# Kernel optimization log

Measured on AMD Instinct MI355X. Metric: run time of the kernel, lower is better.

Reference implementation:

```python
import jax, jax.numpy as jnp
import numpy as np

NUM_SPARSE = 26
VOCAB = 100000
EMB = 64
B = 2048
DENSE = 13
NUM_FEA = NUM_SPARSE + 1  # 26 embeddings + bottom-MLP output


def _xavier(key, shape):
    fan_in, fan_out = shape[0], shape[1]
    lim = jnp.sqrt(6.0 / (fan_in + fan_out))
    return jax.random.uniform(key, shape, jnp.float32, -lim, lim)


def setup_inputs() -> dict:
    key = jax.random.key(0)
    ks = jax.random.split(key, 20)
    inp = {
        "dense": jax.random.normal(ks[0], (B, DENSE), jnp.float32),
        "cat_idx": jax.random.randint(ks[1], (B, NUM_SPARSE), 0, VOCAB, jnp.int32),
        # stacked EmbeddingBag tables (all same vocab -> one [26, V, 64] tensor)
        "tables": _xavier(ks[2], (VOCAB, EMB))[None] * jnp.ones((NUM_SPARSE, 1, 1), jnp.float32) * 0
                  + jax.random.normal(ks[3], (NUM_SPARSE, VOCAB, EMB), jnp.float32) * 0.01,
        # bottom MLP: 13 -> 512 -> 256 -> 64
        "bw0": _xavier(ks[4], (DENSE, 512)), "bb0": jnp.zeros((512,), jnp.float32),
        "bw1": _xavier(ks[5], (512, 256)),   "bb1": jnp.zeros((256,), jnp.float32),
        "bw2": _xavier(ks[6], (256, EMB)),   "bb2": jnp.zeros((EMB,), jnp.float32),
        # top MLP: 415 -> 1024 -> 512 -> 256 -> 1
        "tw0": _xavier(ks[7], (EMB + NUM_FEA * (NUM_FEA - 1) // 2, 1024)), "tb0": jnp.zeros((1024,), jnp.float32),
        "tw1": _xavier(ks[8], (1024, 512)),  "tb1": jnp.zeros((512,), jnp.float32),
        "tw2": _xavier(ks[9], (512, 256)),   "tb2": jnp.zeros((256,), jnp.float32),
        "tw3": _xavier(ks[10], (256, 1)),    "tb3": jnp.zeros((1,), jnp.float32),
    }
    return inp


def reference(dense, cat_idx, tables, bw0, bb0, bw1, bb1, bw2, bb2,
              tw0, tb0, tw1, tb1, tw2, tb2, tw3, tb3):
    # bottom MLP on dense features -> [B, EMB]
    h = jax.nn.relu(dense @ bw0 + bb0)
    h = jax.nn.relu(h @ bw1 + bb1)
    bot = jax.nn.relu(h @ bw2 + bb2)

    # EmbeddingBag (single index per bag, sum mode == plain gather): [B, 26, EMB]
    feat_ids = jnp.arange(NUM_SPARSE)[None, :]  # [1, 26]
    emb = tables[feat_ids, cat_idx]             # [B, 26, EMB]

    # dot interaction: batched Gram matrix then lower-triangular gather
    T = jnp.concatenate([bot[:, None, :], emb], axis=1)  # [B, 27, EMB]
    Z = jnp.einsum("bif,bjf->bij", T, T)                  # [B, 27, 27]
    li, lj = np.tril_indices(NUM_FEA, k=-1)               # 351 pairs
    Zflat = Z[:, li, lj]                                  # [B, 351]

    R = jnp.concatenate([bot, Zflat], axis=1)             # [B, 415]

    # top MLP
    r = jax.nn.relu(R @ tw0 + tb0)
    r = jax.nn.relu(r @ tw1 + tb1)
    r = jax.nn.relu(r @ tw2 + tb2)
    out = jax.nn.sigmoid(r @ tw3 + tb3)                   # [B, 1]
    return out
```

## Files before the change

kernel.cpp:

```cpp
#include <hip/hip_runtime.h>
#include <hip/hip_bf16.h>


#define BATCH 2048
#define VOCAB 100000
#define NSPARSE 26
#define NFEA 27
#define NPAIR 351
#define RLD 512

typedef __attribute__((ext_vector_type(8))) __bf16 bf16x8;
typedef __attribute__((ext_vector_type(4))) float f32x4;
typedef __hip_bfloat16 bf16;

#define GLOAD16(g, l)                                                          \
    __builtin_amdgcn_global_load_lds(                                          \
        (const __attribute__((address_space(1))) unsigned int*)(g),            \
        (__attribute__((address_space(3))) unsigned int*)(l), 16, 0, 0)

template<int BK>
__device__ __forceinline__ int swz(int row, int s) {
    return (BK == 128) ? (s ^ (row & 15))
         : (BK == 64)  ? (s ^ (row & 7))
                       : (s ^ ((row >> 1) & 3));
}

template<int BK, int WR, int WC, int MREP, int NREP, bool DENSEPAD>
__global__ __launch_bounds__(256) void gemm_bf16(
    const void* __restrict__ Araw,
    const bf16* __restrict__ Wt,
    const float* __restrict__ bias,
    bf16* __restrict__ C,
    int M, int N, int K, int ldC)
{
    constexpr int BM    = WR * MREP * 16;
    constexpr int BN    = WC * NREP * 16;
    constexpr int ROWB  = BK * 2;
    constexpr int SLOTS = BK / 8;
    constexpr int KKS   = BK / 32;
    constexpr int PA    = BM * SLOTS / 256;
    constexpr int PB    = BN * SLOTS / 256;

    __shared__ __align__(16) bf16 As[BM * BK];
    __shared__ __align__(16) bf16 Bs[BN * BK];

    const int t   = threadIdx.x;
    const int nbn = N / BN;
    const int bm  = blockIdx.x / nbn;
    const int bn  = blockIdx.x % nbn;
    const int row0 = bm * BM, n0 = bn * BN;

    const int wid  = t >> 6, lane = t & 63;
    const int wr   = wid / WC, wc = wid % WC;
    const int lr   = lane & 15;
    const int q    = lane >> 4;
    const int sslot = t % SLOTS;

    const bf16* Ab[PA];
    const bf16* Bb[PB];
#pragma unroll
    for (int p = 0; p < PA; ++p) {
        const int r = (p * 256 + t) / SLOTS;
        if (!DENSEPAD)
            Ab[p] = (const bf16*)Araw + (size_t)(row0 + r) * K +
                    swz<BK>(r, sslot) * 8;
    }
#pragma unroll
    for (int p = 0; p < PB; ++p) {
        const int r = (p * 256 + t) / SLOTS;
        Bb[p] = Wt + (size_t)(n0 + r) * K + swz<BK>(r, sslot) * 8;
    }

    f32x4 acc[MREP][NREP] = {};

    for (int k0 = 0; k0 < K; k0 += BK) {
        if constexpr (DENSEPAD) {
            const float* Df = (const float*)Araw;
#pragma unroll
            for (int idx = t; idx < BM * 32; idx += 256) {
                const int r = idx >> 5, c = idx & 31;
                const float v = (c < 13) ? Df[(size_t)(row0 + r) * 13 + c] : 0.f;
                As[r * 32 + swz<32>(r, c >> 3) * 8 + (c & 7)] =
                    __float2bfloat16(v);
            }
        } else {
#pragma unroll
            for (int p = 0; p < PA; ++p)
                GLOAD16(Ab[p] + k0, (char*)As + (p * 256 + t) * 16);
        }
#pragma unroll
        for (int p = 0; p < PB; ++p)
            GLOAD16(Bb[p] + k0, (char*)Bs + (p * 256 + t) * 16);
        __syncthreads();

        bf16x8 af[KKS][MREP], bfr[KKS][NREP];
#pragma unroll
        for (int kk = 0; kk < KKS; ++kk) {
#pragma unroll
            for (int m = 0; m < MREP; ++m) {
                const int r = wr * MREP * 16 + 16 * m + lr;
                af[kk][m] = *(const bf16x8*)((const char*)As + r * ROWB +
                                             swz<BK>(r, kk * 4 + q) * 16);
            }
#pragma unroll
            for (int n = 0; n < NREP; ++n) {
                const int r = wc * NREP * 16 + 16 * n + lr;
                bfr[kk][n] = *(const bf16x8*)((const char*)Bs + r * ROWB +
                                              swz<BK>(r, kk * 4 + q) * 16);
            }
        }
#pragma unroll
        for (int kk = 0; kk < KKS; ++kk)
#pragma unroll
            for (int m = 0; m < MREP; ++m)
#pragma unroll
                for (int n = 0; n < NREP; ++n)
                    acc[m][n] = __builtin_amdgcn_mfma_f32_16x16x32_bf16(
                        af[kk][m], bfr[kk][n], acc[m][n], 0, 0, 0);
        __syncthreads();
    }

#pragma unroll
    for (int n = 0; n < NREP; ++n) {
        const int col = n0 + wc * NREP * 16 + 16 * n + lr;
        const float bv = bias[col];
#pragma unroll
        for (int m = 0; m < MREP; ++m) {
#pragma unroll
            for (int i = 0; i < 4; ++i) {
                const int row = row0 + wr * MREP * 16 + 16 * m + q * 4 + i;
                float v = fmaxf(acc[m][n][i] + bv, 0.f);
                C[(size_t)row * ldC + col] = __float2bfloat16(v);
            }
        }
    }
}

__global__ __launch_bounds__(256) void top2_kernel(
    const bf16* __restrict__ A,
    const bf16* __restrict__ Wt,
    const float* __restrict__ bias,
    const float* __restrict__ w3,
    const float* __restrict__ b3,
    float* __restrict__ out)
{
    constexpr int BK = 64, BM = 32, BN = 256, K = 512;
    constexpr int SLOTS = 8, KKS = 2, PA = 1, PB = 8;

    __shared__ __align__(16) bf16 As[BM * BK];
    __shared__ __align__(16) bf16 Bs[BN * BK];
    __shared__ float rsum[BM];

    const int t = threadIdx.x;
    const int row0 = blockIdx.x * BM;
    const int wc = t >> 6, lane = t & 63;
    const int lr = lane & 15, q = lane >> 4;
    const int sslot = t % SLOTS;

    const bf16* Ab[PA];
    const bf16* Bb[PB];
#pragma unroll
    for (int p = 0; p < PA; ++p) {
        const int r = (p * 256 + t) / SLOTS;
        Ab[p] = A + (size_t)(row0 + r) * K + swz<BK>(r, sslot) * 8;
    }
#pragma unroll
    for (int p = 0; p < PB; ++p) {
        const int r = (p * 256 + t) / SLOTS;
        Bb[p] = Wt + (size_t)r * K + swz<BK>(r, sslot) * 8;
    }

    f32x4 acc[2][4] = {};

    for (int k0 = 0; k0 < K; k0 += BK) {
#pragma unroll
        for (int p = 0; p < PA; ++p)
            GLOAD16(Ab[p] + k0, (char*)As + (p * 256 + t) * 16);
#pragma unroll
        for (int p = 0; p < PB; ++p)
            GLOAD16(Bb[p] + k0, (char*)Bs + (p * 256 + t) * 16);
        __syncthreads();

        bf16x8 af[KKS][2], bfr[KKS][4];
#pragma unroll
        for (int kk = 0; kk < KKS; ++kk) {
#pragma unroll
            for (int m = 0; m < 2; ++m) {
                const int r = 16 * m + lr;
                af[kk][m] = *(const bf16x8*)((const char*)As + r * 128 +
                                             swz<BK>(r, kk * 4 + q) * 16);
            }
#pragma unroll
            for (int n = 0; n < 4; ++n) {
                const int r = wc * 64 + 16 * n + lr;
                bfr[kk][n] = *(const bf16x8*)((const char*)Bs + r * 128 +
                                              swz<BK>(r, kk * 4 + q) * 16);
            }
        }
#pragma unroll
        for (int kk = 0; kk < KKS; ++kk)
#pragma unroll
            for (int m = 0; m < 2; ++m)
#pragma unroll
                for (int n = 0; n < 4; ++n)
                    acc[m][n] = __builtin_amdgcn_mfma_f32_16x16x32_bf16(
                        af[kk][m], bfr[kk][n], acc[m][n], 0, 0, 0);
        __syncthreads();
    }

    if (t < BM) rsum[t] = 0.f;
    __syncthreads();

#pragma unroll
    for (int m = 0; m < 2; ++m) {
#pragma unroll
        for (int i = 0; i < 4; ++i) {
            float val = 0.f;
#pragma unroll
            for (int n = 0; n < 4; ++n) {
                const int col = wc * 64 + 16 * n + lr;
                val += fmaxf(acc[m][n][i] + bias[col], 0.f) * w3[col];
            }
            val += __shfl_xor(val, 1);
            val += __shfl_xor(val, 2);
            val += __shfl_xor(val, 4);
            val += __shfl_xor(val, 8);
            if (lr == 0) atomicAdd(&rsum[16 * m + q * 4 + i], val);
        }
    }
    __syncthreads();
    if (t < BM)
        out[row0 + t] = 1.f / (1.f + expf(-(rsum[t] + b3[0])));
}

struct WConvArgs {
    const float* src[6];
    bf16*        dst[6];
    int K[6], N[6], Kp[6], t0[7];
};

__global__ __launch_bounds__(256) void wconv_kernel(WConvArgs a)
{
    __shared__ float Ts[32][33];
    int w = 0;
    while (w < 5 && (int)blockIdx.x >= a.t0[w + 1]) ++w;
    const int rel = blockIdx.x - a.t0[w];
    const int K = a.K[w], N = a.N[w], Kp = a.Kp[w];
    const int nbn = N >> 5;
    const int tk = rel / nbn, tn = rel % nbn;
    const int tx = threadIdx.x & 31, ty = threadIdx.x >> 5;

    const float* src = a.src[w];
    bf16* dst = a.dst[w];

#pragma unroll
    for (int rr = 0; rr < 4; ++rr) {
        const int k = tk * 32 + ty + rr * 8;
        const int n = tn * 32 + tx;
        Ts[ty + rr * 8][tx] = (k < K) ? src[(size_t)k * N + n] : 0.f;
    }
    __syncthreads();
#pragma unroll
    for (int rr = 0; rr < 4; ++rr) {
        const int n = tn * 32 + ty + rr * 8;
        const int kp = tk * 32 + tx;
        dst[(size_t)n * Kp + kp] = __float2bfloat16(Ts[tx][ty + rr * 8]);
    }
}

__global__ __launch_bounds__(256) void interact_kernel(
    const int* __restrict__ cat_idx, const float* __restrict__ tables,
    bf16* __restrict__ R)
{
    __shared__ float T[NFEA][64 + 1];

    const int b    = blockIdx.x;
    const int t    = threadIdx.x;
    const int g    = t >> 6;
    const int lane = t & 63;
    bf16* Rrow = R + (size_t)b * RLD;

    for (int f = g; f < NFEA; f += 4) {
        if (f == 0) {
            T[0][lane] = __bfloat162float(Rrow[lane]);
        } else {
            const int j   = f - 1;
            const int idx = cat_idx[b * NSPARSE + j];
            T[f][lane] = tables[((size_t)j * VOCAB + idx) * 64 + lane];
        }
    }
    __syncthreads();

    if (t < RLD - 415) Rrow[415 + t] = __float2bfloat16(0.f);

    for (int p = t; p < NPAIR; p += 256) {
        int i = (int)((1.0f + sqrtf(1.0f + 8.0f * (float)p)) * 0.5f);
        while (i * (i - 1) / 2 > p) --i;
        while ((i + 1) * i / 2 <= p) ++i;
        const int j = p - i * (i - 1) / 2;
        float s = 0.f;
#pragma unroll 16
        for (int k = 0; k < 64; ++k) s += T[i][k] * T[j][k];
        Rrow[64 + p] = __float2bfloat16(s);
    }
}

extern "C" void kernel_launch(void* const* d_in, const int* in_sizes, int n_in,
                              void* d_out, int out_size, void* d_ws, size_t ws_size,
                              hipStream_t stream)
{
    const float* dense   = (const float*)d_in[0];
    const int*   cat_idx = (const int*)  d_in[1];
    const float* tables  = (const float*)d_in[2];
    const float* bw0 = (const float*)d_in[3];
    const float* bb0 = (const float*)d_in[4];
    const float* bw1 = (const float*)d_in[5];
    const float* bb1 = (const float*)d_in[6];
    const float* bw2 = (const float*)d_in[7];
    const float* bb2 = (const float*)d_in[8];
    const float* tw0 = (const float*)d_in[9];
    const float* tb0 = (const float*)d_in[10];
    const float* tw1 = (const float*)d_in[11];
    const float* tb1 = (const float*)d_in[12];
    const float* tw2 = (const float*)d_in[13];
    const float* tb2 = (const float*)d_in[14];
    const float* tw3 = (const float*)d_in[15];
    const float* tb3 = (const float*)d_in[16];

    bf16* p = (bf16*)d_ws;
    bf16* h0   = p; p += (size_t)BATCH * 512;
    bf16* h1   = p; p += (size_t)BATCH * 256;
    bf16* R    = p; p += (size_t)BATCH * RLD;
    bf16* r0   = p; p += (size_t)BATCH * 1024;
    bf16* r1   = p; p += (size_t)BATCH * 512;
    bf16* bw0t = p; p += 512 * 32;
    bf16* bw1t = p; p += 256 * 512;
    bf16* bw2t = p; p += 64 * 256;
    bf16* tw0t = p; p += 1024 * RLD;
    bf16* tw1t = p; p += 512 * 1024;
    bf16* tw2t = p; p += 256 * 512;
    float* out = (float*)d_out;

    WConvArgs wa;
    wa.src[0] = bw0;  wa.dst[0] = bw0t; wa.K[0] = 13;   wa.N[0] = 512;  wa.Kp[0] = 32;
    wa.src[1] = bw1;  wa.dst[1] = bw1t; wa.K[1] = 512;  wa.N[1] = 256;  wa.Kp[1] = 512;
    wa.src[2] = bw2;  wa.dst[2] = bw2t; wa.K[2] = 256;  wa.N[2] = 64;   wa.Kp[2] = 256;
    wa.src[3] = tw0;  wa.dst[3] = tw0t; wa.K[3] = 415;  wa.N[3] = 1024; wa.Kp[3] = RLD;
    wa.src[4] = tw1;  wa.dst[4] = tw1t; wa.K[4] = 1024; wa.N[4] = 512;  wa.Kp[4] = 1024;
    wa.src[5] = tw2;  wa.dst[5] = tw2t; wa.K[5] = 512;  wa.N[5] = 256;  wa.Kp[5] = 512;
    int tiles = 0;
    for (int w = 0; w < 6; ++w) {
        wa.t0[w] = tiles;
        tiles += (wa.Kp[w] >> 5) * (wa.N[w] >> 5);
    }
    wa.t0[6] = tiles;

    wconv_kernel<<<tiles, 256, 0, stream>>>(wa);

    gemm_bf16<32, 2, 2, 2, 2, true ><<<(BATCH / 64) * (512 / 64), 256, 0, stream>>>(
        dense, bw0t, bb0, h0, BATCH, 512, 32, 512);
    gemm_bf16<128, 2, 2, 2, 2, false><<<(BATCH / 64) * (256 / 64), 256, 0, stream>>>(
        h0, bw1t, bb1, h1, BATCH, 256, 512, 256);
    gemm_bf16<128, 2, 2, 2, 2, false><<<(BATCH / 64) * (64 / 64), 256, 0, stream>>>(
        h1, bw2t, bb2, R, BATCH, 64, 256, RLD);

    interact_kernel<<<BATCH, 256, 0, stream>>>(cat_idx, tables, R);

    gemm_bf16<128, 2, 2, 2, 2, false><<<(BATCH / 64) * (1024 / 64), 256, 0, stream>>>(
        R, tw0t, tb0, r0, BATCH, 1024, RLD, 1024);
    gemm_bf16<128, 2, 2, 2, 2, false><<<(BATCH / 64) * (512 / 64), 256, 0, stream>>>(
        r0, tw1t, tb1, r1, BATCH, 512, 1024, 512);
    top2_kernel<<<BATCH / 32, 256, 0, stream>>>(r1, tw2t, tb2, tw3, tb3, out);
}
```

Before: 63.75 us.

## Merge gather, weight conversion and first bottom GEMM into one multi-role kernel

```diff
diff --git a/kernel.cpp b/kernel.cpp
--- a/kernel.cpp
+++ b/kernel.cpp
@@ -25,12 +25,205 @@
                        : (s ^ ((row >> 1) & 3));
 }
 
-template<int BK, int WR, int WC, int MREP, int NREP, bool DENSEPAD>
+struct Mix1Args {
+    const int* cat; const float* tables; bf16* R; bf16* Tg;
+    const float* wsrc[5]; bf16* wdst[5];
+    int wK[5], wN[5], wKp[5], wt0[6];
+    const float* dense; const float* bw0; const float* bb0; bf16* h0;
+};
+
+__device__ void gather_role(const Mix1Args& a, char* ldsc, int gb)
+{
+    float (*T)[NFEA][65] = (float(*)[NFEA][65])ldsc;
+    const int t  = threadIdx.x;
+    const int b0 = gb * 4;
+
+    for (int l = t; l < 4 * NSPARSE * 16; l += 256) {
+        const int r = l / (NSPARSE * 16), rem = l % (NSPARSE * 16);
+        const int j = rem >> 4, c = (rem & 15) * 4;
+        const int idx = a.cat[(b0 + r) * NSPARSE + j];
+        const float4 v =
+            *(const float4*)&a.tables[((size_t)j * VOCAB + idx) * 64 + c];
+        float* dst = &T[r][j + 1][c];
+        dst[0] = v.x; dst[1] = v.y; dst[2] = v.z; dst[3] = v.w;
+    }
+    for (int z = t; z < 4 * (RLD - 415); z += 256) {
+        const int r = z / (RLD - 415), c = z % (RLD - 415);
+        a.R[(size_t)(b0 + r) * RLD + 415 + c] = __float2bfloat16(0.f);
+    }
+    __syncthreads();
+
+    for (int l = t; l < 4 * NSPARSE * 8; l += 256) {
+        const int r = l / (NSPARSE * 8), rem = l % (NSPARSE * 8);
+        const int j = rem >> 3, k8 = rem & 7;
+        union { bf16 h[8]; bf16x8 v; } pk;
+#pragma unroll
+        for (int u = 0; u < 8; ++u)
+            pk.h[u] = __float2bfloat16(T[r][j + 1][k8 * 8 + u]);
+        *(bf16x8*)&a.Tg[((size_t)(b0 + r) * NSPARSE + j) * 64 + k8 * 8] = pk.v;
+    }
+
+    for (int task = t; task < 4 * NPAIR; task += 256) {
+        const int r = task / NPAIR, p = task % NPAIR;
+        int i = (int)((1.0f + sqrtf(1.0f + 8.0f * (float)p)) * 0.5f);
+        while (i * (i - 1) / 2 > p) --i;
+        while ((i + 1) * i / 2 <= p) ++i;
+        const int j = p - i * (i - 1) / 2;
+        if (j == 0) continue;
+        float s = 0.f;
+#pragma unroll 16
+        for (int k = 0; k < 64; ++k) s += T[r][i][k] * T[r][j][k];
+        a.R[(size_t)(b0 + r) * RLD + 64 + p] = __float2bfloat16(s);
+    }
+}
+
+__device__ void wconv_role(const Mix1Args& a, char* ldsc, int wb)
+{
+    float (*Ts)[33] = (float(*)[33])ldsc;
+    int w = 0;
+    while (w < 4 && wb >= a.wt0[w + 1]) ++w;
+    const int rel = wb - a.wt0[w];
+    const int K = a.wK[w], N = a.wN[w], Kp = a.wKp[w];
+    const int nbn = N >> 5;
+    const int tk = rel / nbn, tn = rel % nbn;
+    const int tx = threadIdx.x & 31, ty = threadIdx.x >> 5;
+
+    const float* src = a.wsrc[w];
+    bf16* dst = a.wdst[w];
+#pragma unroll
+    for (int rr = 0; rr < 4; ++rr) {
+        const int k = tk * 32 + ty + rr * 8, n = tn * 32 + tx;
+        Ts[ty + rr * 8][tx] = (k < K) ? src[(size_t)k * N + n] : 0.f;
+    }
+    __syncthreads();
+#pragma unroll
+    for (int rr = 0; rr < 4; ++rr) {
+        const int n = tn * 32 + ty + rr * 8, kp = tk * 32 + tx;
+        dst[(size_t)n * Kp + kp] = __float2bfloat16(Ts[tx][ty + rr * 8]);
+    }
+}
+
+__device__ void gemm0_role(const Mix1Args& a, char* ldsc, int mb)
+{
+    bf16* As = (bf16*)ldsc;
+    bf16* Bs = (bf16*)(ldsc + 4096);
+    constexpr int N = 512;
+
+    const int t = threadIdx.x;
+    const int nbn = N >> 6;
+    const int bm = mb / nbn, bn = mb % nbn;
+    const int row0 = bm << 6, n0 = bn << 6;
+    const int wid = t >> 6, lane = t & 63;
+    const int wr = wid >> 1, wc = wid & 1;
+    const int lr = lane & 15, q = lane >> 4;
+
+    for (int idx = t; idx < 64 * 32; idx += 256) {
+        const int r = idx >> 5, c = idx & 31;
+        const float v = (c < 13) ? a.dense[(size_t)(row0 + r) * 13 + c] : 0.f;
+        As[r * 32 + swz<32>(r, c >> 3) * 8 + (c & 7)] = __float2bfloat16(v);
+    }
+    for (int idx = t; idx < 64 * 32; idx += 256) {
+        const int r = idx >> 5, c = idx & 31;
+        const float v = (c < 13) ? a.bw0[(size_t)c * N + n0 + r] : 0.f;
+        Bs[r * 32 + swz<32>(r, c >> 3) * 8 + (c & 7)] = __float2bfloat16(v);
+    }
+    __syncthreads();
+
+    f32x4 acc[2][2] = {};
+    bf16x8 af[2], bfr[2];
+#pragma unroll
+    for (int m = 0; m < 2; ++m) {
+        const int r = wr * 32 + 16 * m + lr;
+        af[m] = *(const bf16x8*)((const char*)As + r * 64 + swz<32>(r, q) * 16);
+    }
+#pragma unroll
+    for (int n = 0; n < 2; ++n) {
+        const int r = wc * 32 + 16 * n + lr;
+        bfr[n] = *(const bf16x8*)((const char*)Bs + r * 64 + swz<32>(r, q) * 16);
+    }
+#pragma unroll
+    for (int m = 0; m < 2; ++m)
+#pragma unroll
+        for (int n = 0; n < 2; ++n)
+            acc[m][n] = __builtin_amdgcn_mfma_f32_16x16x32_bf16(
+                af[m], bfr[n], acc[m][n], 0, 0, 0);
+
+#pragma unroll
+    for (int n = 0; n < 2; ++n) {
+        const int col = n0 + wc * 32 + 16 * n + lr;
+        const float bv = a.bb0[col];
+#pragma unroll
+        for (int m = 0; m < 2; ++m) {
+#pragma unroll
+            for (int i = 0; i < 4; ++i) {
+                const int row = row0 + wr * 32 + 16 * m + q * 4 + i;
+                a.h0[(size_t)row * 512 + col] =
+                    __float2bfloat16(fmaxf(acc[m][n][i] + bv, 0.f));
+            }
+        }
+    }
+}
+
+__global__ __launch_bounds__(256) void mix1_kernel(Mix1Args a)
+{
+    __shared__ __align__(16) char lds[28288];
+    const int bid = blockIdx.x;
+    if (bid < 512)            gather_role(a, lds, bid);
+    else if (bid < 1808)      wconv_role(a, lds, bid - 512);
+    else                      gemm0_role(a, lds, bid - 1808);
+}
+
+__global__ __launch_bounds__(256) void botmix_kernel(
+    const bf16* __restrict__ h1, const bf16* __restrict__ bw2t,
+    const float* __restrict__ bb2, const bf16* __restrict__ Tg,
+    bf16* __restrict__ R)
+{
+    __shared__ bf16  h1s[8][256];
+    __shared__ float bots[8][64];
+    const int t  = threadIdx.x;
+    const int b0 = blockIdx.x * 8;
+
+    {   const int r = t >> 5, c = (t & 31) * 8;
+        *(bf16x8*)&h1s[r][c] = *(const bf16x8*)&h1[(size_t)(b0 + r) * 256 + c]; }
+    __syncthreads();
+
+    for (int o = t; o < 512; o += 256) {
+        const int r = o >> 6, n = o & 63;
+        float s = bb2[n];
+        const bf16* wrow = bw2t + (size_t)n * 256;
+#pragma unroll 8
+        for (int k = 0; k < 256; k += 8) {
+            const bf16x8 hv = *(const bf16x8*)&h1s[r][k];
+            const bf16x8 wv = *(const bf16x8*)&wrow[k];
+#pragma unroll
+            for (int u = 0; u < 8; ++u)
+                s += (float)hv[u] * (float)wv[u];
+        }
+        s = fmaxf(s, 0.f);
+        bots[r][n] = s;
+        R[(size_t)(b0 + r) * RLD + n] = __float2bfloat16(s);
+    }
+    __syncthreads();
+
+    if (t < 8 * NSPARSE) {
+        const int r = t / NSPARSE, iz = t % NSPARSE, i = iz + 1;
+        const bf16* tgrow = Tg + ((size_t)(b0 + r) * NSPARSE + iz) * 64;
+        float s = 0.f;
+#pragma unroll
+        for (int k8 = 0; k8 < 8; ++k8) {
+            const bf16x8 ev = *(const bf16x8*)&tgrow[k8 * 8];
+#pragma unroll
+            for (int u = 0; u < 8; ++u)
+                s += (float)ev[u] * bots[r][k8 * 8 + u];
+        }
+        R[(size_t)(b0 + r) * RLD + 64 + i * (i - 1) / 2] = __float2bfloat16(s);
+    }
+}
+
+template<int BK, int WR, int WC, int MREP, int NREP>
 __global__ __launch_bounds__(256) void gemm_bf16(
-    const void* __restrict__ Araw,
-    const bf16* __restrict__ Wt,
-    const float* __restrict__ bias,
-    bf16* __restrict__ C,
+    const bf16* __restrict__ A, const bf16* __restrict__ Wt,
+    const float* __restrict__ bias, bf16* __restrict__ C,
     int M, int N, int K, int ldC)
 {
     constexpr int BM    = WR * MREP * 16;
@@ -61,9 +254,7 @@
 #pragma unroll
     for (int p = 0; p < PA; ++p) {
         const int r = (p * 256 + t) / SLOTS;
-        if (!DENSEPAD)
-            Ab[p] = (const bf16*)Araw + (size_t)(row0 + r) * K +
-                    swz<BK>(r, sslot) * 8;
+        Ab[p] = A + (size_t)(row0 + r) * K + swz<BK>(r, sslot) * 8;
     }
 #pragma unroll
     for (int p = 0; p < PB; ++p) {
@@ -74,20 +265,9 @@
     f32x4 acc[MREP][NREP] = {};
 
     for (int k0 = 0; k0 < K; k0 += BK) {
-        if constexpr (DENSEPAD) {
-            const float* Df = (const float*)Araw;
-#pragma unroll
-            for (int idx = t; idx < BM * 32; idx += 256) {
-                const int r = idx >> 5, c = idx & 31;
-                const float v = (c < 13) ? Df[(size_t)(row0 + r) * 13 + c] : 0.f;
-                As[r * 32 + swz<32>(r, c >> 3) * 8 + (c & 7)] =
-                    __float2bfloat16(v);
-            }
-        } else {
-#pragma unroll
-            for (int p = 0; p < PA; ++p)
-                GLOAD16(Ab[p] + k0, (char*)As + (p * 256 + t) * 16);
-        }
+#pragma unroll
+        for (int p = 0; p < PA; ++p)
+            GLOAD16(Ab[p] + k0, (char*)As + (p * 256 + t) * 16);
 #pragma unroll
         for (int p = 0; p < PB; ++p)
             GLOAD16(Bb[p] + k0, (char*)Bs + (p * 256 + t) * 16);
@@ -129,26 +309,23 @@
 #pragma unroll
             for (int i = 0; i < 4; ++i) {
                 const int row = row0 + wr * MREP * 16 + 16 * m + q * 4 + i;
-                float v = fmaxf(acc[m][n][i] + bv, 0.f);
-                C[(size_t)row * ldC + col] = __float2bfloat16(v);
+                C[(size_t)row * ldC + col] =
+                    __float2bfloat16(fmaxf(acc[m][n][i] + bv, 0.f));
             }
         }
     }
 }
 
 __global__ __launch_bounds__(256) void top2_kernel(
-    const bf16* __restrict__ A,
-    const bf16* __restrict__ Wt,
-    const float* __restrict__ bias,
-    const float* __restrict__ w3,
-    const float* __restrict__ b3,
-    float* __restrict__ out)
-{
-    constexpr int BK = 64, BM = 32, BN = 256, K = 512;
+    const bf16* __restrict__ A, const bf16* __restrict__ Wt,
+    const float* __restrict__ bias, const float* __restrict__ w3,
+    const float* __restrict__ b3, float* __restrict__ out)
+{
+    constexpr int BK = 64, BM = 32, K = 512;
     constexpr int SLOTS = 8, KKS = 2, PA = 1, PB = 8;
 
     __shared__ __align__(16) bf16 As[BM * BK];
-    __shared__ __align__(16) bf16 Bs[BN * BK];
+    __shared__ __align__(16) bf16 Bs[256 * BK];
     __shared__ float rsum[BM];
 
     const int t = threadIdx.x;
@@ -231,78 +408,6 @@
     __syncthreads();
     if (t < BM)
         out[row0 + t] = 1.f / (1.f + expf(-(rsum[t] + b3[0])));
-}
-
-struct WConvArgs {
-    const float* src[6];
-    bf16*        dst[6];
-    int K[6], N[6], Kp[6], t0[7];
-};
-
-__global__ __launch_bounds__(256) void wconv_kernel(WConvArgs a)
-{
-    __shared__ float Ts[32][33];
-    int w = 0;
-    while (w < 5 && (int)blockIdx.x >= a.t0[w + 1]) ++w;
-    const int rel = blockIdx.x - a.t0[w];
-    const int K = a.K[w], N = a.N[w], Kp = a.Kp[w];
-    const int nbn = N >> 5;
-    const int tk = rel / nbn, tn = rel % nbn;
-    const int tx = threadIdx.x & 31, ty = threadIdx.x >> 5;
-
-    const float* src = a.src[w];
-    bf16* dst = a.dst[w];
-
-#pragma unroll
-    for (int rr = 0; rr < 4; ++rr) {
-        const int k = tk * 32 + ty + rr * 8;
-        const int n = tn * 32 + tx;
-        Ts[ty + rr * 8][tx] = (k < K) ? src[(size_t)k * N + n] : 0.f;
-    }
-    __syncthreads();
-#pragma unroll
-    for (int rr = 0; rr < 4; ++rr) {
-        const int n = tn * 32 + ty + rr * 8;
-        const int kp = tk * 32 + tx;
-        dst[(size_t)n * Kp + kp] = __float2bfloat16(Ts[tx][ty + rr * 8]);
-    }
-}
-
-__global__ __launch_bounds__(256) void interact_kernel(
-    const int* __restrict__ cat_idx, const float* __restrict__ tables,
-    bf16* __restrict__ R)
-{
-    __shared__ float T[NFEA][64 + 1];
-
-    const int b    = blockIdx.x;
-    const int t    = threadIdx.x;
-    const int g    = t >> 6;
-    const int lane = t & 63;
-    bf16* Rrow = R + (size_t)b * RLD;
-
-    for (int f = g; f < NFEA; f += 4) {
-        if (f == 0) {
-            T[0][lane] = __bfloat162float(Rrow[lane]);
-        } else {
-            const int j   = f - 1;
-            const int idx = cat_idx[b * NSPARSE + j];
-            T[f][lane] = tables[((size_t)j * VOCAB + idx) * 64 + lane];
-        }
-    }
-    __syncthreads();
-
-    if (t < RLD - 415) Rrow[415 + t] = __float2bfloat16(0.f);
-
-    for (int p = t; p < NPAIR; p += 256) {
-        int i = (int)((1.0f + sqrtf(1.0f + 8.0f * (float)p)) * 0.5f);
-        while (i * (i - 1) / 2 > p) --i;
-        while ((i + 1) * i / 2 <= p) ++i;
-        const int j = p - i * (i - 1) / 2;
-        float s = 0.f;
-#pragma unroll 16
-        for (int k = 0; k < 64; ++k) s += T[i][k] * T[j][k];
-        Rrow[64 + p] = __float2bfloat16(s);
-    }
 }
 
 extern "C" void kernel_launch(void* const* d_in, const int* in_sizes, int n_in,
@@ -333,7 +438,7 @@
     bf16* R    = p; p += (size_t)BATCH * RLD;
     bf16* r0   = p; p += (size_t)BATCH * 1024;
     bf16* r1   = p; p += (size_t)BATCH * 512;
-    bf16* bw0t = p; p += 512 * 32;
+    bf16* Tg   = p; p += (size_t)BATCH * NSPARSE * 64;
     bf16* bw1t = p; p += 256 * 512;
     bf16* bw2t = p; p += 64 * 256;
     bf16* tw0t = p; p += 1024 * RLD;
@@ -341,34 +446,33 @@
     bf16* tw2t = p; p += 256 * 512;
     float* out = (float*)d_out;
 
-    WConvArgs wa;
-    wa.src[0] = bw0;  wa.dst[0] = bw0t; wa.K[0] = 13;   wa.N[0] = 512;  wa.Kp[0] = 32;
-    wa.src[1] = bw1;  wa.dst[1] = bw1t; wa.K[1] = 512;  wa.N[1] = 256;  wa.Kp[1] = 512;
-    wa.src[2] = bw2;  wa.dst[2] = bw2t; wa.K[2] = 256;  wa.N[2] = 64;   wa.Kp[2] = 256;
-    wa.src[3] = tw0;  wa.dst[3] = tw0t; wa.K[3] = 415;  wa.N[3] = 1024; wa.Kp[3] = RLD;
-    wa.src[4] = tw1;  wa.dst[4] = tw1t; wa.K[4] = 1024; wa.N[4] = 512;  wa.Kp[4] = 1024;
-    wa.src[5] = tw2;  wa.dst[5] = tw2t; wa.K[5] = 512;  wa.N[5] = 256;  wa.Kp[5] = 512;
+    Mix1Args ma;
+    ma.cat = cat_idx; ma.tables = tables; ma.R = R; ma.Tg = Tg;
+    ma.wsrc[0] = bw1; ma.wdst[0] = bw1t; ma.wK[0] = 512;  ma.wN[0] = 256;  ma.wKp[0] = 512;
+    ma.wsrc[1] = bw2; ma.wdst[1] = bw2t; ma.wK[1] = 256;  ma.wN[1] = 64;   ma.wKp[1] = 256;
+    ma.wsrc[2] = tw0; ma.wdst[2] = tw0t; ma.wK[2] = 415;  ma.wN[2] = 1024; ma.wKp[2] = RLD;
+    ma.wsrc[3] = tw1; ma.wdst[3] = tw1t; ma.wK[3] = 1024; ma.wN[3] = 512;  ma.wKp[3] = 1024;
+    ma.wsrc[4] = tw2; ma.wdst[4] = tw2t; ma.wK[4] = 512;  ma.wN[4] = 256;  ma.wKp[4] = 512;
     int tiles = 0;
-    for (int w = 0; w < 6; ++w) {
-        wa.t0[w] = tiles;
-        tiles += (wa.Kp[w] >> 5) * (wa.N[w] >> 5);
-    }
-    wa.t0[6] = tiles;
-
-    wconv_kernel<<<tiles, 256, 0, stream>>>(wa);
-
-    gemm_bf16<32, 2, 2, 2, 2, true ><<<(BATCH / 64) * (512 / 64), 256, 0, stream>>>(
-        dense, bw0t, bb0, h0, BATCH, 512, 32, 512);
-    gemm_bf16<128, 2, 2, 2, 2, false><<<(BATCH / 64) * (256 / 64), 256, 0, stream>>>(
+    for (int w = 0; w < 5; ++w) {
+        ma.wt0[w] = tiles;
+        tiles += (ma.wKp[w] >> 5) * (ma.wN[w] >> 5);
+    }
+    ma.wt0[5] = tiles;
+    ma.dense = dense; ma.bw0 = bw0; ma.bb0 = bb0; ma.h0 = h0;
+
+    mix1_kernel<<<512 + tiles + 256, 256, 0, stream>>>(ma);
+
+    gemm_bf16<128, 2, 2, 2, 2><<<(BATCH / 64) * (256 / 64), 256, 0, stream>>>(
         h0, bw1t, bb1, h1, BATCH, 256, 512, 256);
-    gemm_bf16<128, 2, 2, 2, 2, false><<<(BATCH / 64) * (64 / 64), 256, 0, stream>>>(
-        h1, bw2t, bb2, R, BATCH, 64, 256, RLD);
-
-    interact_kernel<<<BATCH, 256, 0, stream>>>(cat_idx, tables, R);
-
-    gemm_bf16<128, 2, 2, 2, 2, false><<<(BATCH / 64) * (1024 / 64), 256, 0, stream>>>(
+
+    botmix_kernel<<<BATCH / 8, 256, 0, stream>>>(h1, bw2t, bb2, Tg, R);
+
+    gemm_bf16<128, 2, 2, 2, 2><<<(BATCH / 64) * (1024 / 64), 256, 0, stream>>>(
         R, tw0t, tb0, r0, BATCH, 1024, RLD, 1024);
-    gemm_bf16<128, 2, 2, 2, 2, false><<<(BATCH / 64) * (512 / 64), 256, 0, stream>>>(
+
+    gemm_bf16<128, 2, 2, 2, 2><<<(BATCH / 64) * (512 / 64), 256, 0, stream>>>(
         r0, tw1t, tb1, r1, BATCH, 512, 1024, 512);
+
     top2_kernel<<<BATCH / 32, 256, 0, stream>>>(r1, tw2t, tb2, tw3, tb3, out);
 }
```

Result: slower. 66.39 us (+4.1%).
